# Kernel optimization log

Measured on AMD Instinct MI355X. Metric: run time of the kernel, lower is better.

The kernel has to match this reference:

```python
import jax, jax.numpy as jnp
import numpy as np

NQ, NT, D = 8192, 8192, 128
EC, EQ, ET = 262144, 262144, 262144


def seg_softmax(logits, seg, num):
    # numerically stable segment softmax over a 1-D logits vector
    m = jax.ops.segment_max(logits, seg, num_segments=num)
    e = jnp.exp(logits - m[seg])
    s = jax.ops.segment_sum(e, seg, num_segments=num)
    return e / s[seg]


def _linear_params(key, din, dout):
    k1, k2 = jax.random.split(key)
    scale = 1.0 / np.sqrt(din)
    W = jax.random.uniform(k1, (din, dout), minval=-scale, maxval=scale, dtype=jnp.float32)
    b = jax.random.uniform(k2, (dout,), minval=-scale, maxval=scale, dtype=jnp.float32)
    return W, b


def setup_inputs():
    key = jax.random.key(0)
    ks = jax.random.split(key, 20)
    inp = {
        'Xq': jax.random.normal(ks[0], (NQ, D), dtype=jnp.float32),
        'edge_index_q': jax.random.randint(ks[1], (2, EQ), 0, NQ),
        'Xt': jax.random.normal(ks[2], (NT, D), dtype=jnp.float32),
        'edge_index_t': jax.random.randint(ks[3], (2, ET), 0, NT),
        'norm_q': jax.random.uniform(ks[4], (NQ, 1), dtype=jnp.float32),
        'norm_t': jax.random.uniform(ks[5], (NT, 1), dtype=jnp.float32),
        'cross_src': jax.random.randint(ks[6], (EC,), 0, NQ),
        'cross_dst': jax.random.randint(ks[7], (EC,), 0, NT),
        'node_mask': jnp.ones((NQ,), dtype=bool),
        'only_run_inter': 0,
    }
    names_dims = [
        ('ac_q', D, D), ('ac_t', D, D), ('vc_q', D, D), ('vc_t', D, D),
        ('mq', 2 * D, D), ('mt', 3 * D, D),
        ('aq', 2 * D, 1), ('vq', 2 * D, D), ('at', 2 * D, 1), ('vt', 2 * D, D),
    ]
    for i, (nm, din, dout) in enumerate(names_dims):
        W, b = _linear_params(ks[8 + i], din, dout)
        inp['W_' + nm] = W
        inp['b_' + nm] = b
    return inp


def reference(Xq, edge_index_q, Xt, edge_index_t, norm_q, norm_t, cross_src, cross_dst,
              node_mask, only_run_inter,
              W_ac_q, b_ac_q, W_ac_t, b_ac_t, W_vc_q, b_vc_q, W_vc_t, b_vc_t,
              W_mq, b_mq, W_mt, b_mt,
              W_aq, b_aq, W_vq, b_vq, W_at, b_at, W_vt, b_vt):
    elu = jax.nn.elu
    nq, nt, d = Xq.shape[0], Xt.shape[0], Xq.shape[1]

    # cross-graph attention logits: per (u, v) pair, dot of transformed features
    Xq_ac = elu(Xq @ W_ac_q + b_ac_q)
    Xt_ac = elu(Xt @ W_ac_t + b_ac_t)
    att_logits = jnp.sum(Xq_ac[cross_src] * Xt_ac[cross_dst], axis=-1)  # [EC]

    # t2q: aggregate target values into query nodes (faithful to original: values gathered by u indices)
    Xt_vc = elu(Xt @ W_vc_t + b_vc_t)
    att_u = seg_softmax(att_logits, cross_src, nq)[:, None]
    Xt2q = jax.ops.segment_sum(att_u * Xt_vc[cross_src], cross_src, num_segments=nq)
    Xq_merged = jnp.concatenate([Xq, Xt2q], axis=1) @ W_mq + b_mq

    # q2t: aggregate query values into target nodes, plus global query summary Q
    Xq_vc = elu(Xq @ W_vc_q + b_vc_q)
    att_v = seg_softmax(att_logits, cross_dst, nt)[:, None]
    Xq2t = jax.ops.segment_sum(att_v * Xq_vc[cross_src], cross_dst, num_segments=nt)
    Q = jnp.broadcast_to(jnp.mean(Xq, axis=0, keepdims=True), (nt, d))
    Xt_merged = jnp.concatenate([Xt, Xq2t, Q], axis=1) @ W_mt + b_mt

    if only_run_inter:
        return Xq_merged, Xt_merged

    # intra-graph edge-wise gather -> MLP -> softmax-scatter message passing
    msg_t = jnp.concatenate([Xt_merged[edge_index_t[0]], Xt_merged[edge_index_t[1]]], axis=1)  # [ET, 2D]
    a_t = seg_softmax((msg_t @ W_at + b_at)[:, 0], edge_index_t[1], nt)[:, None]
    Xt_out = jax.ops.segment_sum(a_t * (msg_t @ W_vt + b_vt), edge_index_t[1], num_segments=nt)

    msg_q = jnp.concatenate([Xq_merged[edge_index_q[0]], Xq_merged[edge_index_q[1]]], axis=1)  # [EQ, 2D]
    a_q = seg_softmax((msg_q @ W_aq + b_aq)[:, 0], edge_index_q[1], nq)[:, None]
    Xq_out = jax.ops.segment_sum(a_q * (msg_q @ W_vq + b_vq), edge_index_q[1], num_segments=nq)

    return Xq_out, Xt_out
```

## Files before the change

kernel.cpp:

```cpp
#include <hip/hip_runtime.h>
#include <math.h>


#define NBIN 8192
#define NB   128
#define DEGCAP 256

__device__ __forceinline__ float elu1(float x) { return x > 0.f ? x : __expf(x) - 1.f; }

__device__ __forceinline__ unsigned short f2bf(float x) {
    unsigned u = __float_as_uint(x);
    u += 0x7FFF + ((u >> 16) & 1);
    return (unsigned short)(u >> 16);
}
__device__ __forceinline__ float bflo(unsigned u) { return __uint_as_float(u << 16); }
__device__ __forceinline__ float bfhi(unsigned u) { return __uint_as_float(u & 0xFFFF0000u); }

struct GemmJob {
    const float* A0; const float* A1; const int* rowmask1;
    const float* W00; const float* W01;
    const float* W10; const float* W11;
    const float* bias0; const float* bias1;
    float* C0; float* C1;
    unsigned short* Cb0; unsigned short* Cb1;
    int act;
};

__global__ __launch_bounds__(256) void gemm_big(GemmJob j0, GemmJob j1)
{
    const GemmJob j = blockIdx.z ? j1 : j0;
    const int out = blockIdx.y >> 1;
    const int c0 = (blockIdx.y & 1) * 64;
    const int r0 = blockIdx.x * 128;
    __shared__ float As[32][132];
    __shared__ float Ws[32][64];
    const int tid = threadIdx.x;
    const int tr = tid >> 4, tc = tid & 15;
    float acc[8][4] = {};

    const float* A_pass[2] = { j.A0, j.A1 };
    const float* W_pass[2] = { out ? j.W01 : j.W00, out ? j.W11 : j.W10 };

    for (int p = 0; p < 2; ++p) {
        const float* A = A_pass[p];
        if (!A) break;
        const float* W = W_pass[p];
        const int* rm = (p == 1) ? j.rowmask1 : nullptr;
        for (int kc = 0; kc < 4; ++kc) {
            {
                const int k4 = (tid & 7) * 4;
                const int rb = tid >> 3;
                #pragma unroll
                for (int i = 0; i < 4; ++i) {
                    const int r = rb + 32 * i;
                    float4 v = *(const float4*)(A + (size_t)(r0 + r) * 128 + kc * 32 + k4);
                    if (rm && rm[r0 + r] == 0) v = make_float4(0.f, 0.f, 0.f, 0.f);
                    As[k4 + 0][r] = v.x; As[k4 + 1][r] = v.y;
                    As[k4 + 2][r] = v.z; As[k4 + 3][r] = v.w;
                }
                const int cc = (tid & 15) * 4;
                const int kb = tid >> 4;
                #pragma unroll
                for (int i = 0; i < 2; ++i) {
                    const int k = kb + 16 * i;
                    *(float4*)&Ws[k][cc] = *(const float4*)(W + (size_t)(kc * 32 + k) * 128 + c0 + cc);
                }
            }
            __syncthreads();
            #pragma unroll 4
            for (int k = 0; k < 32; ++k) {
                const float4 a0 = *(const float4*)&As[k][tr * 4];
                const float4 a1 = *(const float4*)&As[k][64 + tr * 4];
                const float4 w  = *(const float4*)&Ws[k][tc * 4];
                const float ar[8] = {a0.x, a0.y, a0.z, a0.w, a1.x, a1.y, a1.z, a1.w};
                #pragma unroll
                for (int i = 0; i < 8; ++i) {
                    acc[i][0] = fmaf(ar[i], w.x, acc[i][0]);
                    acc[i][1] = fmaf(ar[i], w.y, acc[i][1]);
                    acc[i][2] = fmaf(ar[i], w.z, acc[i][2]);
                    acc[i][3] = fmaf(ar[i], w.w, acc[i][3]);
                }
            }
            __syncthreads();
        }
    }

    float4 bv = make_float4(0.f, 0.f, 0.f, 0.f);
    const float* bias = out ? j.bias1 : j.bias0;
    if (bias) bv = *(const float4*)(bias + c0 + tc * 4);
    float* C = out ? j.C1 : j.C0;
    unsigned short* Cb = out ? j.Cb1 : j.Cb0;
    #pragma unroll
    for (int i = 0; i < 8; ++i) {
        const int row = r0 + (i >> 2) * 64 + tr * 4 + (i & 3);
        float4 o;
        o.x = acc[i][0] + bv.x; o.y = acc[i][1] + bv.y;
        o.z = acc[i][2] + bv.z; o.w = acc[i][3] + bv.w;
        if (j.act) { o.x = elu1(o.x); o.y = elu1(o.y); o.z = elu1(o.z); o.w = elu1(o.w); }
        if (C) {
            *(float4*)(C + (size_t)row * 128 + c0 + tc * 4) = o;
        } else {
            uint2 pk;
            pk.x = (unsigned)f2bf(o.x) | ((unsigned)f2bf(o.y) << 16);
            pk.y = (unsigned)f2bf(o.z) | ((unsigned)f2bf(o.w) << 16);
            *(uint2*)(Cb + (size_t)row * 128 + c0 + tc * 4) = pk;
        }
    }
}

__global__ void gemv2_kernel(const float* __restrict__ A0, const float* __restrict__ w0,
                             float* __restrict__ o0, int M0,
                             const float* __restrict__ A1, const float* __restrict__ w1,
                             float* __restrict__ o1, int M1)
{
    const int wid = (int)((blockIdx.x * blockDim.x + threadIdx.x) >> 6);
    const int lane = threadIdx.x & 63;
    const float* A; const float* w; float* o; int row;
    if (wid < M0) { A = A0; w = w0; o = o0; row = wid; }
    else if (wid < M0 + M1) { A = A1; w = w1; o = o1; row = wid - M0; }
    else return;
    const float2 a = *(const float2*)(A + (size_t)row * 128 + lane * 2);
    const float2 ww = *(const float2*)(w + lane * 2);
    float p = a.x * ww.x + a.y * ww.y;
    #pragma unroll
    for (int s = 32; s; s >>= 1) p += __shfl_xor(p, s, 64);
    if (lane == 0) o[row] = p;
}

__global__ __launch_bounds__(256) void hist_priv(
    const int* __restrict__ cs, const int* __restrict__ cd,
    const int* __restrict__ et1, const int* __restrict__ eq1,
    int* __restrict__ mask_src, unsigned short* __restrict__ partial,
    int EC, int ET, int EQ)
{
    __shared__ int h[NBIN];
    const int k = blockIdx.x, a = blockIdx.y, tid = threadIdx.x;
    const int* idxs[3] = { cd, et1, eq1 };
    const int Es[3] = { EC, ET, EQ };
    for (int b = tid; b < NBIN; b += 256) h[b] = 0;
    __syncthreads();
    const int E = Es[a];
    const int per = (E + NB - 1) / NB;
    const int lo = k * per;
    const int hi = min(E, lo + per);
    const int* idx = idxs[a];
    for (int e = lo + tid; e < hi; e += 256) {
        atomicAdd(&h[idx[e]], 1);
        if (a == 0) mask_src[cs[e]] = 1;
    }
    __syncthreads();
    unsigned short* P = partial + ((size_t)a * NB + k) * NBIN;
    for (int b = tid; b < NBIN; b += 256) P[b] = (unsigned short)h[b];
}

__global__ void binprefix_kernel(unsigned short* __restrict__ partial, int* __restrict__ cnt)
{
    const int bin = blockIdx.x * 256 + threadIdx.x;
    const int a = blockIdx.y;
    unsigned short* P = partial + (size_t)a * NB * NBIN;
    int s = 0;
    #pragma unroll 4
    for (int k = 0; k < NB; ++k) {
        const int p = P[(size_t)k * NBIN + bin];
        P[(size_t)k * NBIN + bin] = (unsigned short)s;
        s += p;
    }
    cnt[a * NBIN + bin] = s;
}

__global__ __launch_bounds__(1024) void scan3_kernel(const int* __restrict__ cnt, int* __restrict__ offs)
{
    const int b = blockIdx.x;
    const int* c = cnt + (size_t)b * NBIN;
    int* o = offs + (size_t)b * (NBIN + 1);
    __shared__ int sums[1024];
    const int tid = threadIdx.x;
    int loc[8]; int s = 0;
    #pragma unroll
    for (int j = 0; j < 8; ++j) { loc[j] = s; s += c[tid * 8 + j]; }
    sums[tid] = s;
    __syncthreads();
    for (int off = 1; off < 1024; off <<= 1) {
        int v = 0;
        if (tid >= off) v = sums[tid - off];
        __syncthreads();
        sums[tid] += v;
        __syncthreads();
    }
    const int ex = tid ? sums[tid - 1] : 0;
    #pragma unroll
    for (int j = 0; j < 8; ++j) o[tid * 8 + j] = ex + loc[j];
    if (tid == 1023) o[NBIN] = sums[1023];
}

__global__ __launch_bounds__(256) void scatter_det(
    const int* __restrict__ cs, const int* __restrict__ cd,
    const int* __restrict__ et0, const int* __restrict__ et1,
    const int* __restrict__ eq0, const int* __restrict__ eq1,
    const unsigned short* __restrict__ partial, const int* __restrict__ offs,
    int* __restrict__ ids_cd, int* __restrict__ ids_t, int* __restrict__ ids_q,
    int EC, int ET, int EQ)
{
    __shared__ int cur[NBIN];
    const int k = blockIdx.x, a = blockIdx.y, tid = threadIdx.x;
    const int Es[3] = { EC, ET, EQ };
    const int* seg[3] = { cd, et1, eq1 };
    const int* pay[3] = { cs, et0, eq0 };
    int* dst[3] = { ids_cd, ids_t, ids_q };
    const unsigned short* P = partial + ((size_t)a * NB + k) * NBIN;
    const int* off = offs + (size_t)a * (NBIN + 1);
    for (int b = tid; b < NBIN; b += 256) cur[b] = off[b] + (int)P[b];
    __syncthreads();
    const int E = Es[a];
    const int per = (E + NB - 1) / NB;
    const int lo = k * per;
    const int hi = min(E, lo + per);
    const int* sg = seg[a]; const int* pl = pay[a]; int* dd = dst[a];
    for (int e = lo + tid; e < hi; e += 256) {
        const int pos = atomicAdd(&cur[sg[e]], 1);
        dd[pos] = pl[e];
    }
}

__global__ void colsum_kernel(const float* __restrict__ X, float* __restrict__ sum)
{
    const int c = threadIdx.x & 127;
    const int half = threadIdx.x >> 7;
    float s = 0.f;
    #pragma unroll 8
    for (int j = 0; j < 64; ++j) {
        const int r = blockIdx.x * 128 + half + 2 * j;
        s += X[(size_t)r * 128 + c];
    }
    atomicAdd(&sum[c], s);
}

__global__ void mt_extra_kernel(const float* __restrict__ Qsum, const float* __restrict__ Wmt,
                                const float* __restrict__ bmt, float* __restrict__ outv, int M)
{
    const int c = threadIdx.x;
    float acc = bmt[c];
    const float inv = 1.0f / (float)M;
    for (int k = 0; k < 128; ++k)
        acc = fmaf(Qsum[k] * inv, Wmt[(size_t)(256 + k) * 128 + c], acc);
    outv[c] = acc;
}

__device__ __forceinline__ void gather_chunk_bf(
    const unsigned int* __restrict__ rows, int myid, float wv, int rem,
    int half, int cl, float4& acc)
{
    const int npairs = (rem + 1) >> 1;
    int j = 0;
    for (; j + 4 <= npairs; j += 4) {
        const int e0 = 2 * j + half, e1 = e0 + 2, e2 = e0 + 4, e3 = e0 + 6;
        const int s0 = __shfl(myid, e0, 64); const float w0 = __shfl(wv, e0, 64);
        const int s1 = __shfl(myid, e1, 64); const float w1 = __shfl(wv, e1, 64);
        const int s2 = __shfl(myid, e2, 64); const float w2 = __shfl(wv, e2, 64);
        const int s3 = __shfl(myid, e3, 64); const float w3 = __shfl(wv, e3, 64);
        const uint2 v0 = *(const uint2*)(rows + (size_t)s0 * 64 + cl * 2);
        const uint2 v1 = *(const uint2*)(rows + (size_t)s1 * 64 + cl * 2);
        const uint2 v2 = *(const uint2*)(rows + (size_t)s2 * 64 + cl * 2);
        const uint2 v3 = *(const uint2*)(rows + (size_t)s3 * 64 + cl * 2);
        acc.x = fmaf(w0, bflo(v0.x), acc.x); acc.y = fmaf(w0, bfhi(v0.x), acc.y);
        acc.z = fmaf(w0, bflo(v0.y), acc.z); acc.w = fmaf(w0, bfhi(v0.y), acc.w);
        acc.x = fmaf(w1, bflo(v1.x), acc.x); acc.y = fmaf(w1, bfhi(v1.x), acc.y);
        acc.z = fmaf(w1, bflo(v1.y), acc.z); acc.w = fmaf(w1, bfhi(v1.y), acc.w);
        acc.x = fmaf(w2, bflo(v2.x), acc.x); acc.y = fmaf(w2, bfhi(v2.x), acc.y);
        acc.z = fmaf(w2, bflo(v2.y), acc.z); acc.w = fmaf(w2, bfhi(v2.y), acc.w);
        acc.x = fmaf(w3, bflo(v3.x), acc.x); acc.y = fmaf(w3, bfhi(v3.x), acc.y);
        acc.z = fmaf(w3, bflo(v3.y), acc.z); acc.w = fmaf(w3, bfhi(v3.y), acc.w);
    }
    for (; j < npairs; ++j) {
        const int e = 2 * j + half;
        const int sv = __shfl(myid, e, 64); const float we = __shfl(wv, e, 64);
        const uint2 v = *(const uint2*)(rows + (size_t)sv * 64 + cl * 2);
        acc.x = fmaf(we, bflo(v.x), acc.x); acc.y = fmaf(we, bfhi(v.x), acc.y);
        acc.z = fmaf(we, bflo(v.y), acc.z); acc.w = fmaf(we, bfhi(v.y), acc.w);
    }
}

__global__ __launch_bounds__(256) void seg_agg_intra(
    const int* ot, const int* it, const float* nlt, const unsigned int* rt,
    const float* xt, const float* ebt, float* outt,
    const int* oq, const int* iq, const float* nlq, const unsigned int* rq,
    const float* xq, const float* ebq, float* outq, int nseg)
{
    const int* offs; const int* ids; const float* nl; const unsigned int* rows;
    const float* extra; const float* eb; float* out;
    if (blockIdx.y == 0) { offs = ot; ids = it; nl = nlt; rows = rt; extra = xt; eb = ebt; out = outt; }
    else                 { offs = oq; ids = iq; nl = nlq; rows = rq; extra = xq; eb = ebq; out = outq; }
    const int wid = (int)((blockIdx.x * blockDim.x + threadIdx.x) >> 6);
    const int lane = threadIdx.x & 63;
    if (wid >= nseg) return;
    const int lo = offs[wid], hi = offs[wid + 1];
    const int deg = hi - lo;
    if (deg == 0) {
        *(float2*)(out + (size_t)wid * 128 + lane * 2) = make_float2(0.f, 0.f);
        return;
    }
    const int half = lane >> 5, cl = lane & 31;
    float s;
    float4 acc = make_float4(0.f, 0.f, 0.f, 0.f);
    if (deg <= 64) {
        int myid = 0; float l = -3.4e38f;
        if (lane < deg) { myid = ids[lo + lane]; l = nl[myid]; }
        float m = l;
        #pragma unroll
        for (int t = 32; t; t >>= 1) m = fmaxf(m, __shfl_xor(m, t, 64));
        const float wv = (lane < deg) ? __expf(l - m) : 0.f;
        s = wv;
        gather_chunk_bf(rows, myid, wv, deg, half, cl, acc);
    } else {
        float m = -3.4e38f;
        for (int i = lo + lane; i < hi; i += 64) m = fmaxf(m, nl[ids[i]]);
        #pragma unroll
        for (int t = 32; t; t >>= 1) m = fmaxf(m, __shfl_xor(m, t, 64));
        s = 0.f;
        for (int base = lo; base < hi; base += 64) {
            const int rem = min(64, hi - base);
            int myid = 0; float wv = 0.f;
            if (lane < rem) { myid = ids[base + lane]; wv = __expf(nl[myid] - m); }
            s += wv;
            gather_chunk_bf(rows, myid, wv, rem, half, cl, acc);
        }
    }
    #pragma unroll
    for (int t = 32; t; t >>= 1) s += __shfl_xor(s, t, 64);
    acc.x += __shfl_xor(acc.x, 32, 64); acc.y += __shfl_xor(acc.y, 32, 64);
    acc.z += __shfl_xor(acc.z, 32, 64); acc.w += __shfl_xor(acc.w, 32, 64);
    if (half == 0) {
        const float inv = 1.f / s;
        const float4 xv = *(const float4*)(extra + (size_t)wid * 128 + cl * 4);
        const float4 bv = *(const float4*)(eb + cl * 4);
        float4 o;
        o.x = fmaf(acc.x, inv, xv.x + bv.x);
        o.y = fmaf(acc.y, inv, xv.y + bv.y);
        o.z = fmaf(acc.z, inv, xv.z + bv.z);
        o.w = fmaf(acc.w, inv, xv.w + bv.w);
        *(float4*)(out + (size_t)wid * 128 + cl * 4) = o;
    }
}

__global__ __launch_bounds__(256) void seg_agg_cross(
    const int* __restrict__ offs, const int* __restrict__ ids,
    const float* __restrict__ Aq, const float* __restrict__ At,
    const unsigned int* __restrict__ Vqb, float* __restrict__ out, int nseg)
{
    __shared__ float atrow[4][128];
    __shared__ float lcache[4][DEGCAP];
    const int w = threadIdx.x >> 6;
    const int lane = threadIdx.x & 63;
    const int wid = blockIdx.x * 4 + w;
    if (wid >= nseg) return;
    const int lo = offs[wid], hi = offs[wid + 1];
    const int deg = hi - lo;
    if (deg == 0) {
        *(float2*)(out + (size_t)wid * 128 + lane * 2) = make_float2(0.f, 0.f);
        return;
    }
    *(float2*)&atrow[w][lane * 2] = *(const float2*)(At + (size_t)wid * 128 + lane * 2);
    __threadfence_block();

    const int half = lane >> 5, cl = lane & 31;
    float s;
    float4 acc = make_float4(0.f, 0.f, 0.f, 0.f);

    if (deg <= 64) {
        int myid = 0; float d = -3.4e38f;
        if (lane < deg) {
            myid = ids[lo + lane];
            const float* ar = Aq + (size_t)myid * 128;
            d = 0.f;
            #pragma unroll 8
            for (int k = 0; k < 128; k += 4) {
                const float4 a = *(const float4*)(ar + k);
                const float4 b = *(const float4*)&atrow[w][k];
                d = fmaf(a.x, b.x, fmaf(a.y, b.y, fmaf(a.z, b.z, fmaf(a.w, b.w, d))));
            }
        }
        float m = d;
        #pragma unroll
        for (int t = 32; t; t >>= 1) m = fmaxf(m, __shfl_xor(m, t, 64));
        const float wv = (lane < deg) ? __expf(d - m) : 0.f;
        s = wv;
        gather_chunk_bf(Vqb, myid, wv, deg, half, cl, acc);
    } else {
        float m = -3.4e38f;
        for (int base = lo; base < hi; base += 64) {
            const int i = base + lane;
            if (i < hi) {
                const int src = ids[i];
                const float* ar = Aq + (size_t)src * 128;
                float d = 0.f;
                #pragma unroll 8
                for (int k = 0; k < 128; k += 4) {
                    const float4 a = *(const float4*)(ar + k);
                    const float4 b = *(const float4*)&atrow[w][k];
                    d = fmaf(a.x, b.x, fmaf(a.y, b.y, fmaf(a.z, b.z, fmaf(a.w, b.w, d))));
                }
                const int li = i - lo;
                if (li < DEGCAP) lcache[w][li] = d;
                m = fmaxf(m, d);
            }
        }
        #pragma unroll
        for (int t = 32; t; t >>= 1) m = fmaxf(m, __shfl_xor(m, t, 64));
        __threadfence_block();
        s = 0.f;
        for (int base = lo; base < hi; base += 64) {
            const int rem = min(64, hi - base);
            int myid = 0; float wv = 0.f;
            if (lane < rem) {
                myid = ids[base + lane];
                const int li = base - lo + lane;
                float d;
                if (li < DEGCAP) d = lcache[w][li];
                else {
                    const float* ar = Aq + (size_t)myid * 128;
                    d = 0.f;
                    for (int k = 0; k < 128; k += 4) {
                        const float4 a = *(const float4*)(ar + k);
                        const float4 b = *(const float4*)&atrow[w][k];
                        d = fmaf(a.x, b.x, fmaf(a.y, b.y, fmaf(a.z, b.z, fmaf(a.w, b.w, d))));
                    }
                }
                wv = __expf(d - m);
            }
            s += wv;
            gather_chunk_bf(Vqb, myid, wv, rem, half, cl, acc);
        }
    }
    #pragma unroll
    for (int t = 32; t; t >>= 1) s += __shfl_xor(s, t, 64);
    acc.x += __shfl_xor(acc.x, 32, 64); acc.y += __shfl_xor(acc.y, 32, 64);
    acc.z += __shfl_xor(acc.z, 32, 64); acc.w += __shfl_xor(acc.w, 32, 64);
    if (half == 0) {
        const float inv = 1.f / s;
        float4 o;
        o.x = acc.x * inv; o.y = acc.y * inv; o.z = acc.z * inv; o.w = acc.w * inv;
        *(float4*)(out + (size_t)wid * 128 + cl * 4) = o;
    }
}

extern "C" void kernel_launch(void* const* d_in, const int* in_sizes, int n_in,
                              void* d_out, int out_size, void* d_ws, size_t ws_size,
                              hipStream_t stream)
{
    const float* Xq    = (const float*)d_in[0];
    const int*   eqidx = (const int*)d_in[1];
    const float* Xt    = (const float*)d_in[2];
    const int*   etidx = (const int*)d_in[3];
    const int*   cs    = (const int*)d_in[6];
    const int*   cd    = (const int*)d_in[7];
    const float* W_ac_q = (const float*)d_in[10]; const float* b_ac_q = (const float*)d_in[11];
    const float* W_ac_t = (const float*)d_in[12]; const float* b_ac_t = (const float*)d_in[13];
    const float* W_vc_q = (const float*)d_in[14]; const float* b_vc_q = (const float*)d_in[15];
    const float* W_vc_t = (const float*)d_in[16]; const float* b_vc_t = (const float*)d_in[17];
    const float* W_mq   = (const float*)d_in[18]; const float* b_mq   = (const float*)d_in[19];
    const float* W_mt   = (const float*)d_in[20]; const float* b_mt   = (const float*)d_in[21];
    const float* W_aq   = (const float*)d_in[22];
    const float* W_vq   = (const float*)d_in[24]; const float* b_vq   = (const float*)d_in[25];
    const float* W_at   = (const float*)d_in[26];
    const float* W_vt   = (const float*)d_in[28]; const float* b_vt   = (const float*)d_in[29];

    const int NQ = in_sizes[0] / 128;
    const int EQ = in_sizes[1] / 2;
    const int NT = in_sizes[2] / 128;
    const int ET = in_sizes[3] / 2;
    const int EC = in_sizes[6];

    const int* eq0 = eqidx;  const int* eq1 = eqidx + EQ;
    const int* et0 = etidx;  const int* et1 = etidx + ET;

    float* base = (float*)d_ws;
    size_t off = 0;
    auto alloc = [&](size_t n) { float* p = base + off; off += n; return p; };
    float* N0 = alloc((size_t)NQ * 128);
    float* N1 = alloc((size_t)NT * 128);
    float* N2 = alloc((size_t)NQ * 128);
    float* N3 = alloc((size_t)NT * 128);
    float* N4 = alloc((size_t)NT * 128);
    unsigned short* B0 = (unsigned short*)alloc((size_t)NQ * 64);
    unsigned short* B1 = (unsigned short*)alloc((size_t)NT * 64);
    unsigned short* B2 = (unsigned short*)alloc((size_t)NQ * 64);
    float* st0v = alloc((size_t)NT);
    float* sq0v = alloc((size_t)NQ);
    float* mte  = alloc(128);
    int* mask_src = (int*)alloc((size_t)NQ);
    float* Qsum   = alloc(128);
    const size_t zero_bytes = ((size_t)NQ + 128) * 4;
    int* cnt  = (int*)alloc((size_t)3 * NBIN);
    int* offs = (int*)alloc((size_t)3 * (NBIN + 1));
    unsigned short* partial = (unsigned short*)alloc((size_t)3 * NB * NBIN / 2);
    int* ids_cd = (int*)alloc((size_t)EC);
    int* ids_t  = (int*)alloc((size_t)ET);
    int* ids_q  = (int*)alloc((size_t)EQ);

    float* Xq_out = (float*)d_out;
    float* Xt_out = (float*)d_out + (size_t)NQ * 128;

    const int* offs_cd = offs;
    const int* offs_t  = offs + (NBIN + 1);
    const int* offs_q  = offs + 2 * (NBIN + 1);

    hipMemsetAsync(mask_src, 0, zero_bytes, stream);

    hist_priv<<<dim3(NB, 3), 256, 0, stream>>>(cs, cd, et1, eq1, mask_src, partial, EC, ET, EQ);
    binprefix_kernel<<<dim3(NBIN / 256, 3), 256, 0, stream>>>(partial, cnt);
    scan3_kernel<<<3, 1024, 0, stream>>>(cnt, offs);
    scatter_det<<<dim3(NB, 3), 256, 0, stream>>>(cs, cd, et0, et1, eq0, eq1, partial, offs,
                                                 ids_cd, ids_t, ids_q, EC, ET, EQ);

    colsum_kernel<<<NQ / 128, 256, 0, stream>>>(Xq, Qsum);

    GemmJob jq{}, jt{};
    jq.A0 = Xq; jq.W00 = W_ac_q; jq.W01 = W_vc_q; jq.bias0 = b_ac_q; jq.bias1 = b_vc_q;
    jq.C0 = N0; jq.Cb1 = B0; jq.act = 1;
    jt.A0 = Xt; jt.W00 = W_ac_t; jt.W01 = W_vc_t; jt.bias0 = b_ac_t; jt.bias1 = b_vc_t;
    jt.C0 = N1; jt.C1 = N3; jt.act = 1;
    gemm_big<<<dim3(NQ / 128, 4, 2), 256, 0, stream>>>(jq, jt);

    seg_agg_cross<<<(NT + 3) / 4, 256, 0, stream>>>(offs_cd, ids_cd, N0, N1,
                                                    (const unsigned int*)B0, N4, NT);

    mt_extra_kernel<<<1, 128, 0, stream>>>(Qsum, W_mt, b_mt, mte, NQ);

    GemmJob mq{}, mt{};
    mq.A0 = Xq; mq.W00 = W_mq;               mq.A1 = N3; mq.W10 = W_mq + 128 * 128;
    mq.rowmask1 = mask_src; mq.bias0 = b_mq; mq.C0 = N2; mq.act = 0;
    mt.A0 = Xt; mt.W00 = W_mt;               mt.A1 = N4; mt.W10 = W_mt + 128 * 128;
    mt.bias0 = mte; mt.C0 = N1; mt.act = 0;
    gemm_big<<<dim3(NQ / 128, 2, 2), 256, 0, stream>>>(mq, mt);

    gemv2_kernel<<<(NT + NQ) / 4, 256, 0, stream>>>(N1, W_at, st0v, NT, N2, W_aq, sq0v, NQ);

    GemmJob ut{}, uq{};
    ut.A0 = N1; ut.W00 = W_vt; ut.W01 = W_vt + 128 * 128; ut.Cb0 = B1; ut.C1 = Xt_out; ut.act = 0;
    uq.A0 = N2; uq.W00 = W_vq; uq.W01 = W_vq + 128 * 128; uq.Cb0 = B2; uq.C1 = Xq_out; uq.act = 0;
    gemm_big<<<dim3(NT / 128, 4, 2), 256, 0, stream>>>(ut, uq);

    seg_agg_intra<<<dim3((NT + 3) / 4, 2), 256, 0, stream>>>(
        offs_t, ids_t, st0v, (const unsigned int*)B1, Xt_out, b_vt, Xt_out,
        offs_q, ids_q, sq0v, (const unsigned int*)B2, Xq_out, b_vq, Xq_out, NT);
}
```

Baseline: 276.2 us.

## Fuse attention gemv into merge GEMM epilogue and store cross-attn features in fp16

Removes the separate gemv kernel by computing the per-row attention-logit dot product inside the merge GEMM epilogue, using shuffle reductions and atomicAdd into zeroed buffers. The cross-attention feature matrices are now written as fp16, and the segment aggregation computes logits with packed fdot2, which halves the gather traffic. The mt_extra reduction is parallelised over 512 threads and launched earlier. In exchange it adds atomics, lowers logit precision to fp16, and leaves the atomic summation order nondeterministic.

```diff
diff --git a/kernel.cpp b/kernel.cpp
--- a/kernel.cpp
+++ b/kernel.cpp
@@ -5,6 +5,8 @@
 #define NBIN 8192
 #define NB   128
 #define DEGCAP 256
+
+typedef _Float16 h2f __attribute__((ext_vector_type(2)));
 
 __device__ __forceinline__ float elu1(float x) { return x > 0.f ? x : __expf(x) - 1.f; }
 
@@ -15,6 +17,29 @@
 }
 __device__ __forceinline__ float bflo(unsigned u) { return __uint_as_float(u << 16); }
 __device__ __forceinline__ float bfhi(unsigned u) { return __uint_as_float(u & 0xFFFF0000u); }
+__device__ __forceinline__ unsigned short f2h(float x) {
+    return __builtin_bit_cast(unsigned short, (_Float16)x);
+}
+
+__device__ __forceinline__ float dot8_f16(const uint4 a, const uint4 b, float d) {
+#if __has_builtin(__builtin_amdgcn_fdot2)
+    d = __builtin_amdgcn_fdot2(__builtin_bit_cast(h2f, a.x), __builtin_bit_cast(h2f, b.x), d, false);
+    d = __builtin_amdgcn_fdot2(__builtin_bit_cast(h2f, a.y), __builtin_bit_cast(h2f, b.y), d, false);
+    d = __builtin_amdgcn_fdot2(__builtin_bit_cast(h2f, a.z), __builtin_bit_cast(h2f, b.z), d, false);
+    d = __builtin_amdgcn_fdot2(__builtin_bit_cast(h2f, a.w), __builtin_bit_cast(h2f, b.w), d, false);
+#else
+    const unsigned ua[4] = { a.x, a.y, a.z, a.w };
+    const unsigned ub[4] = { b.x, b.y, b.z, b.w };
+    #pragma unroll
+    for (int t = 0; t < 4; ++t) {
+        const h2f ha = __builtin_bit_cast(h2f, ua[t]);
+        const h2f hb = __builtin_bit_cast(h2f, ub[t]);
+        d = fmaf((float)ha.x, (float)hb.x, d);
+        d = fmaf((float)ha.y, (float)hb.y, d);
+    }
+#endif
+    return d;
+}
 
 struct GemmJob {
     const float* A0; const float* A1; const int* rowmask1;
@@ -23,6 +48,8 @@
     const float* bias0; const float* bias1;
     float* C0; float* C1;
     unsigned short* Cb0; unsigned short* Cb1;
+    unsigned short* Ch0; unsigned short* Ch1;
+    const float* gvw; float* gvo;
     int act;
 };
 
@@ -90,6 +117,11 @@
     if (bias) bv = *(const float4*)(bias + c0 + tc * 4);
     float* C = out ? j.C1 : j.C0;
     unsigned short* Cb = out ? j.Cb1 : j.Cb0;
+    unsigned short* Ch = out ? j.Ch1 : j.Ch0;
+    const int dogv = (j.gvw != nullptr) && (out == 0);
+    float4 wv4 = make_float4(0.f, 0.f, 0.f, 0.f);
+    if (dogv) wv4 = *(const float4*)(j.gvw + c0 + tc * 4);
+    float pacc[8];
     #pragma unroll
     for (int i = 0; i < 8; ++i) {
         const int row = r0 + (i >> 2) * 64 + tr * 4 + (i & 3);
@@ -97,34 +129,31 @@
         o.x = acc[i][0] + bv.x; o.y = acc[i][1] + bv.y;
         o.z = acc[i][2] + bv.z; o.w = acc[i][3] + bv.w;
         if (j.act) { o.x = elu1(o.x); o.y = elu1(o.y); o.z = elu1(o.z); o.w = elu1(o.w); }
+        pacc[i] = o.x * wv4.x + o.y * wv4.y + o.z * wv4.z + o.w * wv4.w;
         if (C) {
             *(float4*)(C + (size_t)row * 128 + c0 + tc * 4) = o;
-        } else {
+        } else if (Cb) {
             uint2 pk;
             pk.x = (unsigned)f2bf(o.x) | ((unsigned)f2bf(o.y) << 16);
             pk.y = (unsigned)f2bf(o.z) | ((unsigned)f2bf(o.w) << 16);
             *(uint2*)(Cb + (size_t)row * 128 + c0 + tc * 4) = pk;
-        }
-    }
-}
-
-__global__ void gemv2_kernel(const float* __restrict__ A0, const float* __restrict__ w0,
-                             float* __restrict__ o0, int M0,
-                             const float* __restrict__ A1, const float* __restrict__ w1,
-                             float* __restrict__ o1, int M1)
-{
-    const int wid = (int)((blockIdx.x * blockDim.x + threadIdx.x) >> 6);
-    const int lane = threadIdx.x & 63;
-    const float* A; const float* w; float* o; int row;
-    if (wid < M0) { A = A0; w = w0; o = o0; row = wid; }
-    else if (wid < M0 + M1) { A = A1; w = w1; o = o1; row = wid - M0; }
-    else return;
-    const float2 a = *(const float2*)(A + (size_t)row * 128 + lane * 2);
-    const float2 ww = *(const float2*)(w + lane * 2);
-    float p = a.x * ww.x + a.y * ww.y;
-    #pragma unroll
-    for (int s = 32; s; s >>= 1) p += __shfl_xor(p, s, 64);
-    if (lane == 0) o[row] = p;
+        } else {
+            uint2 pk;
+            pk.x = (unsigned)f2h(o.x) | ((unsigned)f2h(o.y) << 16);
+            pk.y = (unsigned)f2h(o.z) | ((unsigned)f2h(o.w) << 16);
+            *(uint2*)(Ch + (size_t)row * 128 + c0 + tc * 4) = pk;
+        }
+    }
+    if (dogv) {
+        #pragma unroll
+        for (int i = 0; i < 8; ++i) {
+            float p = pacc[i];
+            p += __shfl_xor(p, 1, 64); p += __shfl_xor(p, 2, 64);
+            p += __shfl_xor(p, 4, 64); p += __shfl_xor(p, 8, 64);
+            if (tc == 0)
+                atomicAdd(j.gvo + r0 + (i >> 2) * 64 + tr * 4 + (i & 3), p);
+        }
+    }
 }
 
 __global__ __launch_bounds__(256) void hist_priv(
@@ -235,15 +264,20 @@
     atomicAdd(&sum[c], s);
 }
 
-__global__ void mt_extra_kernel(const float* __restrict__ Qsum, const float* __restrict__ Wmt,
-                                const float* __restrict__ bmt, float* __restrict__ outv, int M)
-{
-    const int c = threadIdx.x;
-    float acc = bmt[c];
+__global__ __launch_bounds__(512) void mt_extra_kernel(
+    const float* __restrict__ Qsum, const float* __restrict__ Wmt,
+    const float* __restrict__ bmt, float* __restrict__ outv, int M)
+{
+    __shared__ float red[4][128];
+    const int c = threadIdx.x & 127, kq = threadIdx.x >> 7;
     const float inv = 1.0f / (float)M;
-    for (int k = 0; k < 128; ++k)
+    float acc = 0.f;
+    #pragma unroll 4
+    for (int k = kq * 32; k < kq * 32 + 32; ++k)
         acc = fmaf(Qsum[k] * inv, Wmt[(size_t)(256 + k) * 128 + c], acc);
-    outv[c] = acc;
+    red[kq][c] = acc;
+    __syncthreads();
+    if (kq == 0) outv[c] = bmt[c] + red[0][c] + red[1][c] + red[2][c] + red[3][c];
 }
 
 __device__ __forceinline__ void gather_chunk_bf(
@@ -344,10 +378,10 @@
 
 __global__ __launch_bounds__(256) void seg_agg_cross(
     const int* __restrict__ offs, const int* __restrict__ ids,
-    const float* __restrict__ Aq, const float* __restrict__ At,
+    const unsigned int* __restrict__ Aqh, const unsigned int* __restrict__ Ath,
     const unsigned int* __restrict__ Vqb, float* __restrict__ out, int nseg)
 {
-    __shared__ float atrow[4][128];
+    __shared__ unsigned int atrowh[4][64];
     __shared__ float lcache[4][DEGCAP];
     const int w = threadIdx.x >> 6;
     const int lane = threadIdx.x & 63;
@@ -359,7 +393,7 @@
         *(float2*)(out + (size_t)wid * 128 + lane * 2) = make_float2(0.f, 0.f);
         return;
     }
-    *(float2*)&atrow[w][lane * 2] = *(const float2*)(At + (size_t)wid * 128 + lane * 2);
+    atrowh[w][lane] = Ath[(size_t)wid * 64 + lane];
     __threadfence_block();
 
     const int half = lane >> 5, cl = lane & 31;
@@ -370,14 +404,11 @@
         int myid = 0; float d = -3.4e38f;
         if (lane < deg) {
             myid = ids[lo + lane];
-            const float* ar = Aq + (size_t)myid * 128;
+            const unsigned int* ar = Aqh + (size_t)myid * 64;
             d = 0.f;
-            #pragma unroll 8
-            for (int k = 0; k < 128; k += 4) {
-                const float4 a = *(const float4*)(ar + k);
-                const float4 b = *(const float4*)&atrow[w][k];
-                d = fmaf(a.x, b.x, fmaf(a.y, b.y, fmaf(a.z, b.z, fmaf(a.w, b.w, d))));
-            }
+            #pragma unroll
+            for (int k = 0; k < 64; k += 4)
+                d = dot8_f16(*(const uint4*)(ar + k), *(const uint4*)&atrowh[w][k], d);
         }
         float m = d;
         #pragma unroll
@@ -391,14 +422,11 @@
             const int i = base + lane;
             if (i < hi) {
                 const int src = ids[i];
-                const float* ar = Aq + (size_t)src * 128;
+                const unsigned int* ar = Aqh + (size_t)src * 64;
                 float d = 0.f;
-                #pragma unroll 8
-                for (int k = 0; k < 128; k += 4) {
-                    const float4 a = *(const float4*)(ar + k);
-                    const float4 b = *(const float4*)&atrow[w][k];
-                    d = fmaf(a.x, b.x, fmaf(a.y, b.y, fmaf(a.z, b.z, fmaf(a.w, b.w, d))));
-                }
+                #pragma unroll
+                for (int k = 0; k < 64; k += 4)
+                    d = dot8_f16(*(const uint4*)(ar + k), *(const uint4*)&atrowh[w][k], d);
                 const int li = i - lo;
                 if (li < DEGCAP) lcache[w][li] = d;
                 m = fmaxf(m, d);
@@ -417,13 +445,10 @@
                 float d;
                 if (li < DEGCAP) d = lcache[w][li];
                 else {
-                    const float* ar = Aq + (size_t)myid * 128;
+                    const unsigned int* ar = Aqh + (size_t)myid * 64;
                     d = 0.f;
-                    for (int k = 0; k < 128; k += 4) {
-                        const float4 a = *(const float4*)(ar + k);
-                        const float4 b = *(const float4*)&atrow[w][k];
-                        d = fmaf(a.x, b.x, fmaf(a.y, b.y, fmaf(a.z, b.z, fmaf(a.w, b.w, d))));
-                    }
+                    for (int k = 0; k < 64; k += 4)
+                        d = dot8_f16(*(const uint4*)(ar + k), *(const uint4*)&atrowh[w][k], d);
                 }
                 wv = __expf(d - m);
             }
@@ -476,20 +501,21 @@
     float* base = (float*)d_ws;
     size_t off = 0;
     auto alloc = [&](size_t n) { float* p = base + off; off += n; return p; };
-    float* N0 = alloc((size_t)NQ * 128);
     float* N1 = alloc((size_t)NT * 128);
     float* N2 = alloc((size_t)NQ * 128);
     float* N3 = alloc((size_t)NT * 128);
     float* N4 = alloc((size_t)NT * 128);
+    unsigned int* A0h = (unsigned int*)alloc((size_t)NQ * 64);
+    unsigned int* A1h = (unsigned int*)alloc((size_t)NT * 64);
     unsigned short* B0 = (unsigned short*)alloc((size_t)NQ * 64);
     unsigned short* B1 = (unsigned short*)alloc((size_t)NT * 64);
     unsigned short* B2 = (unsigned short*)alloc((size_t)NQ * 64);
+    float* mte  = alloc(128);
     float* st0v = alloc((size_t)NT);
     float* sq0v = alloc((size_t)NQ);
-    float* mte  = alloc(128);
     int* mask_src = (int*)alloc((size_t)NQ);
     float* Qsum   = alloc(128);
-    const size_t zero_bytes = ((size_t)NQ + 128) * 4;
+    const size_t zero_bytes = ((size_t)NT + NQ + NQ + 128) * 4;
     int* cnt  = (int*)alloc((size_t)3 * NBIN);
     int* offs = (int*)alloc((size_t)3 * (NBIN + 1));
     unsigned short* partial = (unsigned short*)alloc((size_t)3 * NB * NBIN / 2);
@@ -504,7 +530,7 @@
     const int* offs_t  = offs + (NBIN + 1);
     const int* offs_q  = offs + 2 * (NBIN + 1);
 
-    hipMemsetAsync(mask_src, 0, zero_bytes, stream);
+    hipMemsetAsync(st0v, 0, zero_bytes, stream);
 
     hist_priv<<<dim3(NB, 3), 256, 0, stream>>>(cs, cd, et1, eq1, mask_src, partial, EC, ET, EQ);
     binprefix_kernel<<<dim3(NBIN / 256, 3), 256, 0, stream>>>(partial, cnt);
@@ -513,27 +539,26 @@
                                                  ids_cd, ids_t, ids_q, EC, ET, EQ);
 
     colsum_kernel<<<NQ / 128, 256, 0, stream>>>(Xq, Qsum);
+    mt_extra_kernel<<<1, 512, 0, stream>>>(Qsum, W_mt, b_mt, mte, NQ);
 
     GemmJob jq{}, jt{};
     jq.A0 = Xq; jq.W00 = W_ac_q; jq.W01 = W_vc_q; jq.bias0 = b_ac_q; jq.bias1 = b_vc_q;
-    jq.C0 = N0; jq.Cb1 = B0; jq.act = 1;
+    jq.Ch0 = (unsigned short*)A0h; jq.Cb1 = B0; jq.act = 1;
     jt.A0 = Xt; jt.W00 = W_ac_t; jt.W01 = W_vc_t; jt.bias0 = b_ac_t; jt.bias1 = b_vc_t;
-    jt.C0 = N1; jt.C1 = N3; jt.act = 1;
+    jt.Ch0 = (unsigned short*)A1h; jt.C1 = N3; jt.act = 1;
     gemm_big<<<dim3(NQ / 128, 4, 2), 256, 0, stream>>>(jq, jt);
 
-    seg_agg_cross<<<(NT + 3) / 4, 256, 0, stream>>>(offs_cd, ids_cd, N0, N1,
+    seg_agg_cross<<<(NT + 3) / 4, 256, 0, stream>>>(offs_cd, ids_cd, A0h, A1h,
                                                     (const unsigned int*)B0, N4, NT);
-
-    mt_extra_kernel<<<1, 128, 0, stream>>>(Qsum, W_mt, b_mt, mte, NQ);
 
     GemmJob mq{}, mt{};
     mq.A0 = Xq; mq.W00 = W_mq;               mq.A1 = N3; mq.W10 = W_mq + 128 * 128;
-    mq.rowmask1 = mask_src; mq.bias0 = b_mq; mq.C0 = N2; mq.act = 0;
+    mq.rowmask1 = mask_src; mq.bias0 = b_mq; mq.C0 = N2;
+    mq.gvw = W_aq; mq.gvo = sq0v; mq.act = 0;
     mt.A0 = Xt; mt.W00 = W_mt;               mt.A1 = N4; mt.W10 = W_mt + 128 * 128;
-    mt.bias0 = mte; mt.C0 = N1; mt.act = 0;
+    mt.bias0 = mte; mt.C0 = N1;
+    mt.gvw = W_at; mt.gvo = st0v; mt.act = 0;
     gemm_big<<<dim3(NQ / 128, 2, 2), 256, 0, stream>>>(mq, mt);
-
-    gemv2_kernel<<<(NT + NQ) / 4, 256, 0, stream>>>(N1, W_at, st0v, NT, N2, W_aq, sq0v, NQ);
 
     GemmJob ut{}, uq{};
     ut.A0 = N1; ut.W00 = W_vt; ut.W01 = W_vt + 128 * 128; ut.Cb0 = B1; ut.C1 = Xt_out; ut.act = 0;
```

New measurement: 269.2 us. 1.03x faster.
